# Optimization experiments

Measured on AMD Instinct MI355X. Metric: run time of the kernel, lower is better.

The kernel has to match this reference:

```python
import jax, jax.numpy as jnp
import numpy as np

B, H, W, C = 8, 96, 96, 512
M, D, K = 128, 256, 300


def _make_norm_adj(rng):
    A = (rng.random((M, M)) < 0.1).astype(np.float32)
    A = np.maximum(A, A.T)
    A = A + np.eye(M, dtype=np.float32)
    d = A.sum(axis=1)
    d_inv_sqrt = np.power(d, -0.5)
    d_inv_sqrt[np.isinf(d_inv_sqrt)] = 0.0
    Dm = np.diag(d_inv_sqrt)
    return (Dm @ A @ Dm).astype(np.float32)


def setup_inputs() -> dict:
    key = jax.random.key(0)
    ks = jax.random.split(key, 12)
    rng = np.random.default_rng(0)
    norm_adj = jnp.asarray(_make_norm_adj(rng))
    word_emb = jnp.asarray(rng.standard_normal((M, K)).astype(np.float32))
    s = lambda fan_in: 1.0 / np.sqrt(fan_in)
    return {
        "x": jax.random.normal(ks[0], (B, H, W, C), jnp.float32),
        "norm_adj": norm_adj,
        "word_emb": word_emb,
        "Wv": jax.random.normal(ks[1], (C, M), jnp.float32) * s(C),   # voting 1x1 conv
        "bv": jnp.zeros((M,), jnp.float32),
        "Wt": jax.random.normal(ks[2], (C, D), jnp.float32) * s(C),   # feat 1x1 conv
        "bt": jnp.zeros((D,), jnp.float32),
        "Wg": jax.random.normal(ks[3], (D + K, D), jnp.float32) * s(D + K),  # gcn dense
        "bg": jnp.zeros((D,), jnp.float32),
        "Wql": jax.random.normal(ks[4], (C, D), jnp.float32) * s(C),  # compat_local (no bias)
        "Wkn": jax.random.normal(ks[5], (D, D), jnp.float32) * s(D),  # compat_node (no bias)
        "Wm": jax.random.normal(ks[6], (D, C), jnp.float32) * s(D),   # map_back
        "bm": jnp.zeros((C,), jnp.float32),
    }


def reference(x, norm_adj, word_emb, Wv, bv, Wt, bt, Wg, bg, Wql, Wkn, Wm, bm):
    b, h, w, c = x.shape
    xf = x.reshape(b, h * w, c)                      # [B, N, C], N = H*W
    # 1) Voting: local features -> semantic nodes
    vote = jax.nn.softmax(xf @ Wv + bv, axis=2)      # [B, N, M]
    local = xf @ Wt + bt                             # [B, N, D]
    node = jnp.einsum('bnm,bnd->bmd', vote, local)   # [B, M, D]
    # 2) Reason: GCN over semantic graph
    emb = jnp.broadcast_to(word_emb[None], (b, M, K))
    gcn_in = jnp.concatenate([node, emb], axis=-1)   # [B, M, D+K]
    gcn = gcn_in @ Wg + bg                           # [B, M, D]
    evolved = jax.nn.relu(jnp.einsum('mk,bkd->bmd', norm_adj, gcn))
    # 3) Project back via cross-attention
    query = xf @ Wql                                 # [B, N, D]
    keyv = evolved @ Wkn                             # [B, M, D]
    attn = jax.nn.softmax(jnp.einsum('bnd,bmd->bnm', query, keyv), axis=-1)
    values = evolved @ Wm + bm                       # [B, M, C]
    out_global = jnp.einsum('bnm,bmc->bnc', attn, values).reshape(b, h, w, c)
    return jax.nn.relu(x + out_global)
```

## Files before the change

### kernel.cpp

```cpp
#include <hip/hip_runtime.h>
#include <hip/hip_bf16.h>

#define BB 8
#define NN 9216
#define BN 73728
#define CC 512
#define MM 128
#define DD 256
#define KK 300
#define DK 556
#define PSTR 640

typedef __attribute__((ext_vector_type(8))) __bf16 bf16x8;
typedef __attribute__((ext_vector_type(4))) float f32x4;

__device__ __forceinline__ void lds_load16(const void* g, void* l) {
    __builtin_amdgcn_global_load_lds(
        (const __attribute__((address_space(1))) unsigned int*)g,
        (__attribute__((address_space(3))) unsigned int*)l, 16, 0, 0);
}

__global__ __launch_bounds__(256) void pack_wt(const float* __restrict__ Wv, const float* __restrict__ bv,
                                               const float* __restrict__ Wt, const float* __restrict__ bt,
                                               const float* __restrict__ Wql,
                                               __bf16* __restrict__ WcatT, float* __restrict__ bias) {
    int gid = blockIdx.x * 256 + threadIdx.x;
    if (gid < PSTR * 512) {
        int n = gid >> 9, k = gid & 511;
        float v;
        if (n < 128)       v = Wv[k * 128 + n];
        else if (n < 384)  v = Wt[k * 256 + (n - 128)];
        else               v = Wql[k * 256 + (n - 384)];
        WcatT[gid] = (__bf16)v;
    }
    if (gid < PSTR) {
        bias[gid] = (gid < 128) ? bv[gid] : ((gid < 384) ? bt[gid - 128] : 0.0f);
    }
}

__global__ __launch_bounds__(256) void cast_x(const float* __restrict__ x, __bf16* __restrict__ xb) {
    long total = (long)BN * CC;
    for (long i = ((long)blockIdx.x * 256 + threadIdx.x) * 8; i < total; i += (long)gridDim.x * 256 * 8) {
        float4 a = *(const float4*)&x[i];
        float4 b = *(const float4*)&x[i + 4];
        bf16x8 o;
        o[0] = (__bf16)a.x; o[1] = (__bf16)a.y; o[2] = (__bf16)a.z; o[3] = (__bf16)a.w;
        o[4] = (__bf16)b.x; o[5] = (__bf16)b.y; o[6] = (__bf16)b.z; o[7] = (__bf16)b.w;
        *(bf16x8*)&xb[i] = o;
    }
}

__global__ __launch_bounds__(256, 2) void proj_mfma(const __bf16* __restrict__ xb,
                                                    const __bf16* __restrict__ WcatT,
                                                    const float* __restrict__ bias,
                                                    float* __restrict__ P) {
    __shared__ __align__(16) __bf16 Al[128 * 64];
    __shared__ __align__(16) __bf16 Bl[128 * 64];
    int t = threadIdx.x, w = t >> 6, l = t & 63;
    int lo = l & 15, hi = l >> 4;
    int wr = w >> 1, wc = w & 1;
    int n0 = blockIdx.x * 128;
    long row0 = (long)blockIdx.y * 128;

    f32x4 acc[4][4];
    #pragma unroll
    for (int m = 0; m < 4; m++)
        #pragma unroll
        for (int n = 0; n < 4; n++) acc[m][n] = (f32x4){0.f, 0.f, 0.f, 0.f};

    int lrow = l >> 3, lcol = (l & 7) * 8;
    for (int k0 = 0; k0 < 512; k0 += 64) {
        __syncthreads();
        #pragma unroll
        for (int i = 0; i < 4; i++) {
            int c = w * 4 + i;
            lds_load16(xb + (row0 + c * 8 + lrow) * (long)CC + k0 + lcol,
                       (char*)Al + c * 1024);
            lds_load16(WcatT + (long)(n0 + c * 8 + lrow) * CC + k0 + lcol,
                       (char*)Bl + c * 1024);
        }
        __syncthreads();
        #pragma unroll
        for (int ks = 0; ks < 2; ks++) {
            bf16x8 af[4], bfr[4];
            #pragma unroll
            for (int m = 0; m < 4; m++)
                af[m] = *(const bf16x8*)&Al[(wr * 64 + m * 16 + lo) * 64 + ks * 32 + hi * 8];
            #pragma unroll
            for (int n = 0; n < 4; n++)
                bfr[n] = *(const bf16x8*)&Bl[(wc * 64 + n * 16 + lo) * 64 + ks * 32 + hi * 8];
            #pragma unroll
            for (int m = 0; m < 4; m++)
                #pragma unroll
                for (int n = 0; n < 4; n++)
                    acc[m][n] = __builtin_amdgcn_mfma_f32_16x16x32_bf16(af[m], bfr[n], acc[m][n], 0, 0, 0);
        }
    }

    float bv[4];
    #pragma unroll
    for (int n = 0; n < 4; n++) bv[n] = bias[n0 + wc * 64 + n * 16 + lo];
    #pragma unroll
    for (int m = 0; m < 4; m++)
        #pragma unroll
        for (int n = 0; n < 4; n++)
            #pragma unroll
            for (int r = 0; r < 4; r++) {
                long row = row0 + wr * 64 + m * 16 + hi * 4 + r;
                P[row * PSTR + n0 + wc * 64 + n * 16 + lo] = acc[m][n][r] + bv[n];
            }
}

__global__ __launch_bounds__(256) void softmax_vote(float* __restrict__ P) {
    int wid = threadIdx.x >> 6, lane = threadIdx.x & 63;
    long row = (long)blockIdx.x * 4 + wid;
    float* p = &P[row * PSTR];
    float v0 = p[lane], v1 = p[lane + 64];
    float mx = fmaxf(v0, v1);
    #pragma unroll
    for (int off = 32; off; off >>= 1) mx = fmaxf(mx, __shfl_xor(mx, off));
    float e0 = __expf(v0 - mx), e1 = __expf(v1 - mx);
    float s = e0 + e1;
    #pragma unroll
    for (int off = 32; off; off >>= 1) s += __shfl_xor(s, off);
    float r = 1.0f / s;
    p[lane] = e0 * r;
    p[lane + 64] = e1 * r;
}

__global__ __launch_bounds__(256) void node_gemm(const float* __restrict__ P, float* __restrict__ node) {
    __shared__ float Vs[32][33];
    __shared__ float Ls[32][64];
    int t = threadIdx.x;
    int blk = blockIdx.x;
    int nc = blk & 7, dt = (blk >> 3) & 3, mt = (blk >> 5) & 3, b = blk >> 7;
    int m0 = mt * 32, d0 = dt * 64, nbase = nc * 1152;
    long brow = (long)b * NN;
    int tx = t & 15, ty = t >> 4;
    float acc[2][4] = {};
    for (int nn = 0; nn < 1152; nn += 32) {
        __syncthreads();
        #pragma unroll
        for (int j = 0; j < 4; j++) {
            int idx = j * 256 + t;
            int r = idx >> 5, mm = idx & 31;
            Vs[r][mm] = P[(brow + nbase + nn + r) * PSTR + m0 + mm];
        }
        #pragma unroll
        for (int j = 0; j < 8; j++) {
            int idx = j * 256 + t;
            int r = idx >> 6, dd = idx & 63;
            Ls[r][dd] = P[(brow + nbase + nn + r) * PSTR + 128 + d0 + dd];
        }
        __syncthreads();
        #pragma unroll 8
        for (int n = 0; n < 32; n++) {
            float va[2] = {Vs[n][ty * 2], Vs[n][ty * 2 + 1]};
            float4 vb4 = *(const float4*)&Ls[n][tx * 4];
            float vb[4] = {vb4.x, vb4.y, vb4.z, vb4.w};
            #pragma unroll
            for (int i = 0; i < 2; i++)
                #pragma unroll
                for (int j = 0; j < 4; j++)
                    acc[i][j] += va[i] * vb[j];
        }
    }
    #pragma unroll
    for (int i = 0; i < 2; i++)
        #pragma unroll
        for (int j = 0; j < 4; j++)
            unsafeAtomicAdd(&node[(b * MM + m0 + ty * 2 + i) * DD + d0 + tx * 4 + j], acc[i][j]);
}

__global__ __launch_bounds__(256) void gcn_dense(const float* __restrict__ node, const float* __restrict__ emb,
                                                 const float* __restrict__ Wg, const float* __restrict__ bg,
                                                 float* __restrict__ gcn) {
    __shared__ float a[DK];
    int b = blockIdx.x >> 7, m = blockIdx.x & 127, t = threadIdx.x;
    for (int i = t; i < DK; i += 256)
        a[i] = (i < DD) ? node[(b * MM + m) * DD + i] : emb[m * KK + (i - DD)];
    __syncthreads();
    float acc = bg[t];
    for (int k = 0; k < DK; k++) acc += a[k] * Wg[k * DD + t];
    gcn[(b * MM + m) * DD + t] = acc;
}

__global__ __launch_bounds__(256) void gcn_adj_relu(const float* __restrict__ adj, const float* __restrict__ gcn,
                                                    float* __restrict__ evo) {
    __shared__ float ar[128];
    int b = blockIdx.x >> 7, m = blockIdx.x & 127, t = threadIdx.x;
    if (t < 128) ar[t] = adj[m * MM + t];
    __syncthreads();
    float acc = 0.0f;
    for (int k = 0; k < MM; k++) acc += ar[k] * gcn[(b * MM + k) * DD + t];
    evo[(b * MM + m) * DD + t] = fmaxf(acc, 0.0f);
}

__global__ __launch_bounds__(256) void keyv_k(const float* __restrict__ evo, const float* __restrict__ Wkn,
                                              __bf16* __restrict__ Kbf) {
    __shared__ float e[DD];
    int b = blockIdx.x >> 7, m = blockIdx.x & 127, t = threadIdx.x;
    e[t] = evo[(b * MM + m) * DD + t];
    __syncthreads();
    float acc = 0.0f;
    for (int k = 0; k < DD; k++) acc += e[k] * Wkn[k * DD + t];
    Kbf[(b * MM + m) * DD + t] = (__bf16)acc;
}

__global__ __launch_bounds__(512) void values_k(const float* __restrict__ evo, const float* __restrict__ Wm,
                                                const float* __restrict__ bm, __bf16* __restrict__ Vt) {
    __shared__ float e[DD];
    int b = blockIdx.x >> 7, m = blockIdx.x & 127, t = threadIdx.x;
    if (t < DD) e[t] = evo[(b * MM + m) * DD + t];
    __syncthreads();
    float acc = bm[t];
    for (int k = 0; k < DD; k++) acc += e[k] * Wm[k * CC + t];
    Vt[((long)b * CC + t) * MM + m] = (__bf16)acc;
}

__global__ __launch_bounds__(256, 2) void attn_mfma(const float* __restrict__ P,
                                                    const __bf16* __restrict__ Kbf,
                                                    const __bf16* __restrict__ Vt,
                                                    const float* __restrict__ x,
                                                    float* __restrict__ out) {
    __shared__ __align__(16) __bf16 Pl[4][16][136];
    int t = threadIdx.x;
    int w = t >> 6, l = t & 63;
    int lo = l & 15, hi = l >> 4;
    int b = blockIdx.x / 144, tile = blockIdx.x % 144;
    int n0 = tile * 64;
    long brow = (long)b * NN;
    long qrow = brow + n0 + w * 16 + lo;
    const float* Pq = P + qrow * PSTR + 384;
    const __bf16* Kb = Kbf + (long)b * MM * DD;
    const __bf16* Vb = Vt + (long)b * CC * MM;

    f32x4 S[8];
    #pragma unroll
    for (int i = 0; i < 8; i++) S[i] = (f32x4){0.f, 0.f, 0.f, 0.f};

    #pragma unroll
    for (int k0 = 0; k0 < 8; k0++) {
        float4 qa = *(const float4*)(Pq + k0 * 32 + hi * 8);
        float4 qb = *(const float4*)(Pq + k0 * 32 + hi * 8 + 4);
        bf16x8 A;
        A[0] = (__bf16)qa.x; A[1] = (__bf16)qa.y; A[2] = (__bf16)qa.z; A[3] = (__bf16)qa.w;
        A[4] = (__bf16)qb.x; A[5] = (__bf16)qb.y; A[6] = (__bf16)qb.z; A[7] = (__bf16)qb.w;
        #pragma unroll
        for (int mt = 0; mt < 8; mt++) {
            bf16x8 Bf = *(const bf16x8*)(Kb + (mt * 16 + lo) * DD + k0 * 32 + hi * 8);
            S[mt] = __builtin_amdgcn_mfma_f32_16x16x32_bf16(A, Bf, S[mt], 0, 0, 0);
        }
    }

    float mx[4], sm[4], rs[4];
    #pragma unroll
    for (int r = 0; r < 4; r++) {
        float m0 = S[0][r];
        #pragma unroll
        for (int mt = 1; mt < 8; mt++) m0 = fmaxf(m0, S[mt][r]);
        #pragma unroll
        for (int off = 1; off < 16; off <<= 1) m0 = fmaxf(m0, __shfl_xor(m0, off));
        mx[r] = m0;
    }
    #pragma unroll
    for (int r = 0; r < 4; r++) sm[r] = 0.f;
    #pragma unroll
    for (int mt = 0; mt < 8; mt++)
        #pragma unroll
        for (int r = 0; r < 4; r++) {
            float e = __expf(S[mt][r] - mx[r]);
            S[mt][r] = e;
            sm[r] += e;
        }
    #pragma unroll
    for (int r = 0; r < 4; r++) {
        float s0 = sm[r];
        #pragma unroll
        for (int off = 1; off < 16; off <<= 1) s0 += __shfl_xor(s0, off);
        rs[r] = 1.0f / s0;
    }
    #pragma unroll
    for (int mt = 0; mt < 8; mt++)
        #pragma unroll
        for (int r = 0; r < 4; r++)
            Pl[w][hi * 4 + r][mt * 16 + lo] = (__bf16)(S[mt][r] * rs[r]);

    f32x4 O[32];
    #pragma unroll
    for (int i = 0; i < 32; i++) O[i] = (f32x4){0.f, 0.f, 0.f, 0.f};

    #pragma unroll
    for (int mc = 0; mc < 4; mc++) {
        bf16x8 A2 = *(const bf16x8*)&Pl[w][lo][mc * 32 + hi * 8];
        #pragma unroll
        for (int ct = 0; ct < 32; ct++) {
            bf16x8 Bv = *(const bf16x8*)(Vb + (long)(ct * 16 + lo) * MM + mc * 32 + hi * 8);
            O[ct] = __builtin_amdgcn_mfma_f32_16x16x32_bf16(A2, Bv, O[ct], 0, 0, 0);
        }
    }

    #pragma unroll
    for (int ct = 0; ct < 32; ct++) {
        #pragma unroll
        for (int r = 0; r < 4; r++) {
            long gi = (brow + n0 + w * 16 + hi * 4 + r) * (long)CC + ct * 16 + lo;
            out[gi] = fmaxf(x[gi] + O[ct][r], 0.f);
        }
    }
}

extern "C" void kernel_launch(void* const* d_in, const int* in_sizes, int n_in,
                              void* d_out, int out_size, void* d_ws, size_t ws_size,
                              hipStream_t stream) {
    const float* x    = (const float*)d_in[0];
    const float* adj  = (const float*)d_in[1];
    const float* emb  = (const float*)d_in[2];
    const float* Wv   = (const float*)d_in[3];
    const float* bv   = (const float*)d_in[4];
    const float* Wt   = (const float*)d_in[5];
    const float* bt   = (const float*)d_in[6];
    const float* Wg   = (const float*)d_in[7];
    const float* bg   = (const float*)d_in[8];
    const float* Wql  = (const float*)d_in[9];
    const float* Wkn  = (const float*)d_in[10];
    const float* Wm   = (const float*)d_in[11];
    const float* bm   = (const float*)d_in[12];
    float* out = (float*)d_out;

    float* ws    = (float*)d_ws;
    __bf16* WcatT = (__bf16*)ws;
    float* bias  = (float*)(WcatT + PSTR * 512);
    float* P     = bias + PSTR;
    float* node  = P + (long)BN * PSTR;
    float* gcn   = node + BB * MM * DD;
    float* evo   = gcn + BB * MM * DD;
    __bf16* Kbf  = (__bf16*)(evo + BB * MM * DD);
    __bf16* Vt   = Kbf + (long)BB * MM * DD;
    __bf16* xb   = (__bf16*)d_out;

    pack_wt<<<1280, 256, 0, stream>>>(Wv, bv, Wt, bt, Wql, WcatT, bias);
    cast_x<<<2048, 256, 0, stream>>>(x, xb);
    proj_mfma<<<dim3(5, 576), 256, 0, stream>>>(xb, WcatT, bias, P);
    softmax_vote<<<BN / 4, 256, 0, stream>>>(P);
    hipMemsetAsync(node, 0, (size_t)BB * MM * DD * sizeof(float), stream);
    node_gemm<<<1024, 256, 0, stream>>>(P, node);
    gcn_dense<<<BB * MM, 256, 0, stream>>>(node, emb, Wg, bg, gcn);
    gcn_adj_relu<<<BB * MM, 256, 0, stream>>>(adj, gcn, evo);
    keyv_k<<<BB * MM, 256, 0, stream>>>(evo, Wkn, Kbf);
    values_k<<<BB * MM, 512, 0, stream>>>(evo, Wm, bm, Vt);
    attn_mfma<<<BB * 144, 256, 0, stream>>>(P, Kbf, Vt, x, out);
}
```

Before: 829.5 us.

## Compute vote-local node aggregation with bf16 MFMA and split projection outputs

Replaces the fp32 scalar node_gemm with a bf16 MFMA kernel that transposes vote and local tiles into LDS and reduces per-slice partials with atomics. The projection kernel now writes local features as bf16 into a separate buffer and keeps logits and query in a narrower fp32 array. The softmax writes bf16 votes instead of overwriting in place. This shrinks memory traffic for the intermediate and moves the aggregation onto matrix cores, at the cost of bf16 rounding in node features and uncoalesced strided gather loads during the LDS transpose.

```diff
diff --git a/kernel.cpp b/kernel.cpp
--- a/kernel.cpp
+++ b/kernel.cpp
@@ -9,15 +9,23 @@
 #define DD 256
 #define KK 300
 #define DK 556
-#define PSTR 640
+#define PS 384
 
 typedef __attribute__((ext_vector_type(8))) __bf16 bf16x8;
+typedef __attribute__((ext_vector_type(4))) __bf16 bf16x4;
 typedef __attribute__((ext_vector_type(4))) float f32x4;
 
 __device__ __forceinline__ void lds_load16(const void* g, void* l) {
     __builtin_amdgcn_global_load_lds(
         (const __attribute__((address_space(1))) unsigned int*)g,
         (__attribute__((address_space(3))) unsigned int*)l, 16, 0, 0);
+}
+
+__device__ __forceinline__ bf16x8 combine8(bf16x4 a, bf16x4 b) {
+    bf16x8 r;
+    r[0] = a[0]; r[1] = a[1]; r[2] = a[2]; r[3] = a[3];
+    r[4] = b[0]; r[5] = b[1]; r[6] = b[2]; r[7] = b[3];
+    return r;
 }
 
 __global__ __launch_bounds__(256) void pack_wt(const float* __restrict__ Wv, const float* __restrict__ bv,
@@ -25,7 +33,7 @@
                                                const float* __restrict__ Wql,
                                                __bf16* __restrict__ WcatT, float* __restrict__ bias) {
     int gid = blockIdx.x * 256 + threadIdx.x;
-    if (gid < PSTR * 512) {
+    if (gid < 640 * 512) {
         int n = gid >> 9, k = gid & 511;
         float v;
         if (n < 128)       v = Wv[k * 128 + n];
@@ -33,7 +41,7 @@
         else               v = Wql[k * 256 + (n - 384)];
         WcatT[gid] = (__bf16)v;
     }
-    if (gid < PSTR) {
+    if (gid < 640) {
         bias[gid] = (gid < 128) ? bv[gid] : ((gid < 384) ? bt[gid - 128] : 0.0f);
     }
 }
@@ -53,7 +61,8 @@
 __global__ __launch_bounds__(256, 2) void proj_mfma(const __bf16* __restrict__ xb,
                                                     const __bf16* __restrict__ WcatT,
                                                     const float* __restrict__ bias,
-                                                    float* __restrict__ P) {
+                                                    float* __restrict__ P,
+                                                    __bf16* __restrict__ localbf) {
     __shared__ __align__(16) __bf16 Al[128 * 64];
     __shared__ __align__(16) __bf16 Bl[128 * 64];
     int t = threadIdx.x, w = t >> 6, l = t & 63;
@@ -107,14 +116,18 @@
             #pragma unroll
             for (int r = 0; r < 4; r++) {
                 long row = row0 + wr * 64 + m * 16 + hi * 4 + r;
-                P[row * PSTR + n0 + wc * 64 + n * 16 + lo] = acc[m][n][r] + bv[n];
+                int col = n0 + wc * 64 + n * 16 + lo;
+                float v = acc[m][n][r] + bv[n];
+                if (n0 == 0)           P[row * PS + col] = v;
+                else if (n0 < 384)     localbf[row * 256 + (col - 128)] = (__bf16)v;
+                else                   P[row * PS + (col - 256)] = v;
             }
 }
 
-__global__ __launch_bounds__(256) void softmax_vote(float* __restrict__ P) {
+__global__ __launch_bounds__(256) void softmax_vote(const float* __restrict__ P, __bf16* __restrict__ votebf) {
     int wid = threadIdx.x >> 6, lane = threadIdx.x & 63;
     long row = (long)blockIdx.x * 4 + wid;
-    float* p = &P[row * PSTR];
+    const float* p = &P[row * PS];
     float v0 = p[lane], v1 = p[lane + 64];
     float mx = fmaxf(v0, v1);
     #pragma unroll
@@ -124,52 +137,76 @@
     #pragma unroll
     for (int off = 32; off; off >>= 1) s += __shfl_xor(s, off);
     float r = 1.0f / s;
-    p[lane] = e0 * r;
-    p[lane + 64] = e1 * r;
-}
-
-__global__ __launch_bounds__(256) void node_gemm(const float* __restrict__ P, float* __restrict__ node) {
-    __shared__ float Vs[32][33];
-    __shared__ float Ls[32][64];
-    int t = threadIdx.x;
-    int blk = blockIdx.x;
-    int nc = blk & 7, dt = (blk >> 3) & 3, mt = (blk >> 5) & 3, b = blk >> 7;
-    int m0 = mt * 32, d0 = dt * 64, nbase = nc * 1152;
-    long brow = (long)b * NN;
-    int tx = t & 15, ty = t >> 4;
-    float acc[2][4] = {};
-    for (int nn = 0; nn < 1152; nn += 32) {
+    votebf[row * 128 + lane] = (__bf16)(e0 * r);
+    votebf[row * 128 + lane + 64] = (__bf16)(e1 * r);
+}
+
+__global__ __launch_bounds__(256) void node_mfma(const __bf16* __restrict__ votebf,
+                                                 const __bf16* __restrict__ localbf,
+                                                 float* __restrict__ node) {
+    __shared__ __align__(16) __bf16 Vl[128][68];
+    __shared__ __align__(16) __bf16 Ll[256][68];
+    int t = threadIdx.x, w = t >> 6, l = t & 63;
+    int lo = l & 15, hi = l >> 4;
+    int b = blockIdx.x / 36, slice = blockIdx.x % 36;
+    long base = (long)b * NN + slice * 256;
+
+    f32x4 acc[8][4];
+    #pragma unroll
+    for (int mt = 0; mt < 8; mt++)
+        #pragma unroll
+        for (int dt = 0; dt < 4; dt++) acc[mt][dt] = (f32x4){0.f, 0.f, 0.f, 0.f};
+
+    int mcol = t & 127, qh = t >> 7;
+    for (int c0 = 0; c0 < 256; c0 += 64) {
         __syncthreads();
         #pragma unroll
-        for (int j = 0; j < 4; j++) {
-            int idx = j * 256 + t;
-            int r = idx >> 5, mm = idx & 31;
-            Vs[r][mm] = P[(brow + nbase + nn + r) * PSTR + m0 + mm];
-        }
-        #pragma unroll
         for (int j = 0; j < 8; j++) {
-            int idx = j * 256 + t;
-            int r = idx >> 6, dd = idx & 63;
-            Ls[r][dd] = P[(brow + nbase + nn + r) * PSTR + 128 + d0 + dd];
+            int q = j * 2 + qh;
+            long n = base + c0 + q * 4;
+            bf16x4 pk;
+            pk[0] = votebf[n * 128 + mcol];
+            pk[1] = votebf[(n + 1) * 128 + mcol];
+            pk[2] = votebf[(n + 2) * 128 + mcol];
+            pk[3] = votebf[(n + 3) * 128 + mcol];
+            *(bf16x4*)&Vl[mcol][q * 4] = pk;
+        }
+        #pragma unroll
+        for (int q = 0; q < 16; q++) {
+            long n = base + c0 + q * 4;
+            bf16x4 pk;
+            pk[0] = localbf[n * 256 + t];
+            pk[1] = localbf[(n + 1) * 256 + t];
+            pk[2] = localbf[(n + 2) * 256 + t];
+            pk[3] = localbf[(n + 3) * 256 + t];
+            *(bf16x4*)&Ll[t][q * 4] = pk;
         }
         __syncthreads();
-        #pragma unroll 8
-        for (int n = 0; n < 32; n++) {
-            float va[2] = {Vs[n][ty * 2], Vs[n][ty * 2 + 1]};
-            float4 vb4 = *(const float4*)&Ls[n][tx * 4];
-            float vb[4] = {vb4.x, vb4.y, vb4.z, vb4.w};
-            #pragma unroll
-            for (int i = 0; i < 2; i++)
+        #pragma unroll
+        for (int ks = 0; ks < 2; ks++) {
+            bf16x8 bfr[4];
+            #pragma unroll
+            for (int dt = 0; dt < 4; dt++)
+                bfr[dt] = combine8(*(const bf16x4*)&Ll[w * 64 + dt * 16 + lo][ks * 32 + hi * 8],
+                                   *(const bf16x4*)&Ll[w * 64 + dt * 16 + lo][ks * 32 + hi * 8 + 4]);
+            #pragma unroll
+            for (int mt = 0; mt < 8; mt++) {
+                bf16x8 A = combine8(*(const bf16x4*)&Vl[mt * 16 + lo][ks * 32 + hi * 8],
+                                    *(const bf16x4*)&Vl[mt * 16 + lo][ks * 32 + hi * 8 + 4]);
                 #pragma unroll
-                for (int j = 0; j < 4; j++)
-                    acc[i][j] += va[i] * vb[j];
-        }
-    }
-    #pragma unroll
-    for (int i = 0; i < 2; i++)
-        #pragma unroll
-        for (int j = 0; j < 4; j++)
-            unsafeAtomicAdd(&node[(b * MM + m0 + ty * 2 + i) * DD + d0 + tx * 4 + j], acc[i][j]);
+                for (int dt = 0; dt < 4; dt++)
+                    acc[mt][dt] = __builtin_amdgcn_mfma_f32_16x16x32_bf16(A, bfr[dt], acc[mt][dt], 0, 0, 0);
+            }
+        }
+    }
+    #pragma unroll
+    for (int mt = 0; mt < 8; mt++)
+        #pragma unroll
+        for (int dt = 0; dt < 4; dt++)
+            #pragma unroll
+            for (int r = 0; r < 4; r++)
+                unsafeAtomicAdd(&node[((long)b * MM + mt * 16 + hi * 4 + r) * DD + w * 64 + dt * 16 + lo],
+                                acc[mt][dt][r]);
 }
 
 __global__ __launch_bounds__(256) void gcn_dense(const float* __restrict__ node, const float* __restrict__ emb,
@@ -231,7 +268,7 @@
     int n0 = tile * 64;
     long brow = (long)b * NN;
     long qrow = brow + n0 + w * 16 + lo;
-    const float* Pq = P + qrow * PSTR + 384;
+    const float* Pq = P + qrow * PS + 128;
     const __bf16* Kb = Kbf + (long)b * MM * DD;
     const __bf16* Vb = Vt + (long)b * CC * MM;
 
@@ -328,23 +365,25 @@
     const float* bm   = (const float*)d_in[12];
     float* out = (float*)d_out;
 
-    float* ws    = (float*)d_ws;
-    __bf16* WcatT = (__bf16*)ws;
-    float* bias  = (float*)(WcatT + PSTR * 512);
-    float* P     = bias + PSTR;
-    float* node  = P + (long)BN * PSTR;
-    float* gcn   = node + BB * MM * DD;
-    float* evo   = gcn + BB * MM * DD;
-    __bf16* Kbf  = (__bf16*)(evo + BB * MM * DD);
-    __bf16* Vt   = Kbf + (long)BB * MM * DD;
-    __bf16* xb   = (__bf16*)d_out;
+    float* ws      = (float*)d_ws;
+    __bf16* WcatT  = (__bf16*)ws;
+    float* bias    = (float*)(WcatT + 640 * 512);
+    float* P       = bias + 640;
+    __bf16* localbf = (__bf16*)(P + (long)BN * PS);
+    __bf16* votebf  = localbf + (long)BN * 256;
+    float* node    = (float*)(votebf + (long)BN * 128);
+    float* gcn     = node + BB * MM * DD;
+    float* evo     = gcn + BB * MM * DD;
+    __bf16* Kbf    = (__bf16*)(evo + BB * MM * DD);
+    __bf16* Vt     = Kbf + (long)BB * MM * DD;
+    __bf16* xb     = (__bf16*)d_out;
 
     pack_wt<<<1280, 256, 0, stream>>>(Wv, bv, Wt, bt, Wql, WcatT, bias);
     cast_x<<<2048, 256, 0, stream>>>(x, xb);
-    proj_mfma<<<dim3(5, 576), 256, 0, stream>>>(xb, WcatT, bias, P);
-    softmax_vote<<<BN / 4, 256, 0, stream>>>(P);
+    proj_mfma<<<dim3(5, 576), 256, 0, stream>>>(xb, WcatT, bias, P, localbf);
+    softmax_vote<<<BN / 4, 256, 0, stream>>>(P, votebf);
     hipMemsetAsync(node, 0, (size_t)BB * MM * DD * sizeof(float), stream);
-    node_gemm<<<1024, 256, 0, stream>>>(P, node);
+    node_mfma<<<BB * 36, 256, 0, stream>>>(votebf, localbf, node);
     gcn_dense<<<BB * MM, 256, 0, stream>>>(node, emb, Wg, bg, gcn);
     gcn_adj_relu<<<BB * MM, 256, 0, stream>>>(adj, gcn, evo);
     keyv_k<<<BB * MM, 256, 0, stream>>>(evo, Wkn, Kbf);
```

Result: faster. 694.9 us (-16.2%).
